# Kernel tuning notes

Measured on AMD Instinct MI355X. Metric: run time of the kernel, lower is better.

The kernel has to match this reference:

```python
import jax, jax.numpy as jnp
import numpy as np

B_BATCH, H_DIM, W_DIM, D_MODEL, N_STATE = 4, 64, 64, 512, 8


def setup_inputs() -> dict:
    key = jax.random.key(0)
    ks = jax.random.split(key, 7)
    x = jax.random.normal(ks[0], (B_BATCH, H_DIM * W_DIM, D_MODEL), jnp.float32)
    # stable diagonal recurrence: 0 < A < 1
    A = jax.random.uniform(ks[1], (D_MODEL, N_STATE), jnp.float32, 0.5, 0.99)
    Bm = jax.random.normal(ks[2], (D_MODEL, N_STATE), jnp.float32) * 0.1
    Cm = jax.random.normal(ks[3], (D_MODEL, N_STATE), jnp.float32) * 0.1
    D_skip = jax.random.normal(ks[4], (D_MODEL,), jnp.float32)
    Wp = jax.random.normal(ks[5], (D_MODEL, D_MODEL), jnp.float32) / np.sqrt(D_MODEL)
    b_proj = jnp.zeros((D_MODEL,), jnp.float32)
    return {"x": x, "h": H_DIM, "w": W_DIM, "A": A, "Bm": Bm, "Cm": Cm,
            "D_skip": D_skip, "Wp": Wp, "b_proj": b_proj}


def _ssm(xs, A, Bm, Cm, D_skip):
    # xs: (batch', L, d). Diagonal SSM: s_t = A*s_{t-1} + B*x_t; y_t = C.s_t + D*x_t
    bt, L, d = xs.shape
    n = A.shape[1]

    def step(s, x_t):  # s: (bt, d, n), x_t: (bt, d)
        s = A * s + Bm * x_t[:, :, None]
        y = jnp.einsum('bdn,dn->bd', s, Cm) + D_skip * x_t
        return s, y

    s0 = jnp.zeros((bt, d, n), xs.dtype)
    _, ys = jax.lax.scan(step, s0, jnp.swapaxes(xs, 0, 1))  # ys: (L, bt, d)
    return jnp.swapaxes(ys, 0, 1)


def reference(x, h, w, A, Bm, Cm, D_skip, Wp, b_proj):
    b, l, d = x.shape
    xg = x.reshape(b, h, w, d)
    # horizontal direction: 'b (h w) d -> (b w) h d' -> scan over h
    x_h = jnp.transpose(xg, (0, 2, 1, 3)).reshape(b * w, h, d)
    y_h = _ssm(x_h, A, Bm, Cm, D_skip).reshape(b, w, h, d)
    y_h = jnp.transpose(y_h, (0, 2, 1, 3)).reshape(b, l, d)
    # vertical direction: 'b (h w) d -> (b h) w d' -> scan over w
    x_v = xg.reshape(b * h, w, d)
    y_v = _ssm(x_v, A, Bm, Cm, D_skip).reshape(b, l, d)
    # fused add + output projection (Linear: x @ W.T + b)
    return (y_h + y_v) @ Wp.T + b_proj
```

## Files before the change

### kernel.cpp

```cpp
#include <hip/hip_runtime.h>

#define BB 4
#define HH 64
#define WW 64
#define DD 512
#define NS 8
#define MROWS (BB * HH * WW)

typedef __attribute__((ext_vector_type(8))) __bf16 bf16x8;
typedef __attribute__((ext_vector_type(4))) float f32x4;

__device__ inline short f2bf(float f) {
  unsigned u = __float_as_uint(f);
  return (short)((u + 0x7fff + ((u >> 16) & 1)) >> 16);
}
__device__ inline float bf2f(short s) {
  return __uint_as_float(((unsigned)(unsigned short)s) << 16);
}

__device__ inline float ssm_step(float xv, float* s, const float* a,
                                 const float* bm, const float* cm, float dk) {
#pragma unroll
  for (int n = 0; n < NS; ++n) s[n] = fmaf(a[n], s[n], bm[n] * xv);
  float p0 = s[0] * cm[0], p1 = s[1] * cm[1], p2 = s[2] * cm[2],
        p3 = s[3] * cm[3], p4 = s[4] * cm[4], p5 = s[5] * cm[5],
        p6 = s[6] * cm[6], p7 = s[7] * cm[7];
  float q0 = p0 + p1, q1 = p2 + p3, q2 = p4 + p5, q3 = p6 + p7;
  return fmaf(dk, xv, (q0 + q1) + (q2 + q3));
}

__global__ __launch_bounds__(256) void scan_h_kernel(
    const float* __restrict__ x, const float* __restrict__ A,
    const float* __restrict__ Bm, const float* __restrict__ Cm,
    const float* __restrict__ Dsk, short* __restrict__ y,
    const float* __restrict__ Wp, short* __restrict__ wb) {
  if (blockIdx.x >= 256) {
    const int cid = (blockIdx.x - 256) * 2 + blockIdx.y;
    const int i = (cid * 256 + (int)threadIdx.x) * 8;
    const float4 v0 = *(const float4*)&Wp[i];
    const float4 v1 = *(const float4*)&Wp[i + 4];
    short r[8];
    r[0] = f2bf(v0.x); r[1] = f2bf(v0.y); r[2] = f2bf(v0.z); r[3] = f2bf(v0.w);
    r[4] = f2bf(v1.x); r[5] = f2bf(v1.y); r[6] = f2bf(v1.z); r[7] = f2bf(v1.w);
    *(short4*)&wb[i] = *(short4*)&r[0];
    *(short4*)&wb[i + 4] = *(short4*)&r[4];
    return;
  }

  const int seq = blockIdx.x;
  const int d = blockIdx.y * 256 + threadIdx.x;
  const int b = seq >> 6;
  const int r = seq & 63;

  size_t base = ((size_t)b * HH * WW + r) * DD + d;
  const size_t step = (size_t)WW * DD;

  float a[NS], bm[NS], cm[NS], s[NS];
#pragma unroll
  for (int i = 0; i < NS; i += 4) {
    float4 t;
    t = *(const float4*)&A[(size_t)d * NS + i];
    a[i] = t.x; a[i + 1] = t.y; a[i + 2] = t.z; a[i + 3] = t.w;
    t = *(const float4*)&Bm[(size_t)d * NS + i];
    bm[i] = t.x; bm[i + 1] = t.y; bm[i + 2] = t.z; bm[i + 3] = t.w;
    t = *(const float4*)&Cm[(size_t)d * NS + i];
    cm[i] = t.x; cm[i + 1] = t.y; cm[i + 2] = t.z; cm[i + 3] = t.w;
  }
  const float dk = Dsk[d];
#pragma unroll
  for (int i = 0; i < NS; ++i) s[i] = 0.f;

  float xs[4][8];
#pragma unroll
  for (int i = 0; i < 8; ++i) xs[0][i] = x[base + (size_t)i * step];
#pragma unroll
  for (int i = 0; i < 8; ++i) xs[1][i] = x[base + (size_t)(8 + i) * step];

#pragma unroll 4
  for (int c = 0; c < 8; ++c) {
    const int cur = c & 3;
    if (c < 6) {
      const size_t pbase = base + 16 * step;
#pragma unroll
      for (int i = 0; i < 8; ++i)
        xs[(c + 2) & 3][i] = x[pbase + (size_t)i * step];
    }
#pragma unroll
    for (int i = 0; i < 8; ++i)
      y[base + (size_t)i * step] = f2bf(ssm_step(xs[cur][i], s, a, bm, cm, dk));
    base += 8 * step;
  }
}

__global__ __launch_bounds__(512) void scanv_gemm_kernel(
    const float* __restrict__ x, const float* __restrict__ A,
    const float* __restrict__ Bm, const float* __restrict__ Cm,
    const float* __restrict__ Dsk, const short* __restrict__ yh,
    const short* __restrict__ Wb, const float* __restrict__ bias,
    float* __restrict__ out) {
  __shared__ __align__(16) char LDSBUF[131072];
  short* Ys = (short*)LDSBUF;
  short* Bs0 = (short*)(LDSBUF + 65536);
  short* Bs1 = (short*)(LDSBUF + 98304);

  const int tid = (int)threadIdx.x;
  const int lane = tid & 63;
  const int wid = tid >> 6;
  const int m0 = blockIdx.x * 64;
  const int d = tid;

  auto stageB = [&](int ks, short* bsb) {
    const int k0 = ks * 32;
#pragma unroll
    for (int c = 0; c < 4; ++c) {
      const int chunk = wid * 4 + c;
      const int n = chunk * 16 + (lane >> 2);
      const int kslot = ((lane & 3) ^ (n & 3)) << 3;
      const short* g = &Wb[(size_t)n * DD + k0 + kslot];
      __builtin_amdgcn_global_load_lds(
          (const __attribute__((address_space(1))) unsigned int*)g,
          (__attribute__((address_space(3))) unsigned int*)((char*)bsb +
                                                            chunk * 1024),
          16, 0, 0);
    }
  };

  float a[NS], bm[NS], cm[NS], s[NS];
#pragma unroll
  for (int i = 0; i < NS; i += 4) {
    float4 t;
    t = *(const float4*)&A[(size_t)d * NS + i];
    a[i] = t.x; a[i + 1] = t.y; a[i + 2] = t.z; a[i + 3] = t.w;
    t = *(const float4*)&Bm[(size_t)d * NS + i];
    bm[i] = t.x; bm[i + 1] = t.y; bm[i + 2] = t.z; bm[i + 3] = t.w;
    t = *(const float4*)&Cm[(size_t)d * NS + i];
    cm[i] = t.x; cm[i + 1] = t.y; cm[i + 2] = t.z; cm[i + 3] = t.w;
  }
  const float dk = Dsk[d];
#pragma unroll
  for (int i = 0; i < NS; ++i) s[i] = 0.f;

  size_t base = (size_t)m0 * DD + d;
  stageB(0, Bs0);

  float xs[4][8], yp[4][8];
#pragma unroll
  for (int i = 0; i < 8; ++i) xs[0][i] = x[base + (size_t)i * DD];
#pragma unroll
  for (int i = 0; i < 8; ++i) yp[0][i] = bf2f(yh[base + (size_t)i * DD]);
#pragma unroll
  for (int i = 0; i < 8; ++i) xs[1][i] = x[base + (size_t)(8 + i) * DD];
#pragma unroll
  for (int i = 0; i < 8; ++i) yp[1][i] = bf2f(yh[base + (size_t)(8 + i) * DD]);

#pragma unroll 4
  for (int c = 0; c < 8; ++c) {
    const int cur = c & 3;
    if (c < 6) {
      const size_t pbase = base + 16 * DD;
#pragma unroll
      for (int i = 0; i < 8; ++i)
        xs[(c + 2) & 3][i] = x[pbase + (size_t)i * DD];
#pragma unroll
      for (int i = 0; i < 8; ++i)
        yp[(c + 2) & 3][i] = bf2f(yh[pbase + (size_t)i * DD]);
    }
#pragma unroll
    for (int i = 0; i < 8; ++i) {
      const int w = c * 8 + i;
      const float acc = ssm_step(xs[cur][i], s, a, bm, cm, dk) + yp[cur][i];
      Ys[w * DD + (d ^ ((w & 7) << 3))] = f2bf(acc);
    }
    base += 8 * DD;
  }

  __syncthreads();

  f32x4 acc4[4][4];
#pragma unroll
  for (int m = 0; m < 4; ++m)
#pragma unroll
    for (int n = 0; n < 4; ++n) acc4[m][n] = (f32x4){0.f, 0.f, 0.f, 0.f};

  const int fr = lane & 15;
  const int kfr = (lane >> 4) * 8;

  int cur = 0;
  for (int ks = 0; ks < 16; ++ks) {
    if (ks < 15) {
      stageB(ks + 1, (cur ^ 1) ? Bs1 : Bs0);
      asm volatile("s_waitcnt vmcnt(4)" ::: "memory");
    } else {
      asm volatile("s_waitcnt vmcnt(0)" ::: "memory");
    }
    __builtin_amdgcn_sched_barrier(0);

    const short* bsr = cur ? Bs1 : Bs0;
    bf16x8 af[4], bfv[4];
    const int kg = ks * 32 + kfr;
#pragma unroll
    for (int m = 0; m < 4; ++m) {
      const int r = m * 16 + fr;
      af[m] = *(const bf16x8*)(const void*)&Ys[r * DD + (kg ^ ((r & 7) << 3))];
    }
#pragma unroll
    for (int n = 0; n < 4; ++n) {
      const int nn = wid * 64 + n * 16 + fr;
      bfv[n] = *(const bf16x8*)(const void*)&bsr[nn * 32 +
                                                 (kfr ^ ((nn & 3) << 3))];
    }
    __builtin_amdgcn_s_setprio(1);
#pragma unroll
    for (int m = 0; m < 4; ++m)
#pragma unroll
      for (int n = 0; n < 4; ++n)
        acc4[m][n] = __builtin_amdgcn_mfma_f32_16x16x32_bf16(
            af[m], bfv[n], acc4[m][n], 0, 0, 0);
    __builtin_amdgcn_s_setprio(0);
    __builtin_amdgcn_sched_barrier(0);
    cur ^= 1;
  }

  __syncthreads();
  float* Wt = (float*)(LDSBUF + (size_t)wid * 16384);

  const int c16 = lane & 15;
  float bv[4];
#pragma unroll
  for (int n = 0; n < 4; ++n) bv[n] = bias[wid * 64 + n * 16 + c16];

#pragma unroll
  for (int m = 0; m < 4; ++m)
#pragma unroll
    for (int n = 0; n < 4; ++n)
#pragma unroll
      for (int j = 0; j < 4; ++j) {
        const int row = m * 16 + (lane >> 4) * 4 + j;
        const int col = n * 16 + c16;
        Wt[row * 64 + col] = acc4[m][n][j] + bv[n];
      }
#pragma unroll
  for (int rr = 0; rr < 16; ++rr) {
    const int row = rr * 4 + (lane >> 4);
    const int col4 = c16 * 4;
    const float4 v = *(const float4*)&Wt[row * 64 + col4];
    *(float4*)&out[(size_t)(m0 + row) * DD + wid * 64 + col4] = v;
  }
}

extern "C" void kernel_launch(void* const* d_in, const int* in_sizes, int n_in,
                              void* d_out, int out_size, void* d_ws,
                              size_t ws_size, hipStream_t stream) {
  const float* x = (const float*)d_in[0];
  const float* A = (const float*)d_in[3];
  const float* Bm = (const float*)d_in[4];
  const float* Cm = (const float*)d_in[5];
  const float* Dsk = (const float*)d_in[6];
  const float* Wp = (const float*)d_in[7];
  const float* bpj = (const float*)d_in[8];
  float* out = (float*)d_out;

  short* yh = (short*)d_ws;
  short* wb = (short*)((char*)d_ws + (size_t)MROWS * DD * 2);

  const dim3 grid_h(256 + 64, DD / 256);
  scan_h_kernel<<<grid_h, 256, 0, stream>>>(x, A, Bm, Cm, Dsk, yh, Wp, wb);

  scanv_gemm_kernel<<<BB * HH, 512, 0, stream>>>(x, A, Bm, Cm, Dsk, yh, wb,
                                                 bpj, out);
}
```

Baseline: 42.33 us.

## Split vertical scan into two halves with carry correction, double block threads

The fused vertical-scan+GEMM kernel now runs 1024 threads per block. Two thread groups each scan half of the 64-step row from a zero state. The second half is then corrected by adding C·(A^k·s_carry) from the first group's final state, passed through LDS. This halves the serial scan latency per block. The GEMM is re-tiled so each of 16 waves computes 64x32 outputs, and results are stored directly to global without the LDS transpose. The costs are an extra correction pass, a second bf16 rounding of the affected Ys entries, and uncoalesced scalar output stores. The priority hints are also removed.

```diff
diff --git a/kernel.cpp b/kernel.cpp
--- a/kernel.cpp
+++ b/kernel.cpp
@@ -92,7 +92,7 @@
   }
 }
 
-__global__ __launch_bounds__(512) void scanv_gemm_kernel(
+__global__ __launch_bounds__(1024) void scanv_gemm_kernel(
     const float* __restrict__ x, const float* __restrict__ A,
     const float* __restrict__ Bm, const float* __restrict__ Cm,
     const float* __restrict__ Dsk, const short* __restrict__ yh,
@@ -102,18 +102,20 @@
   short* Ys = (short*)LDSBUF;
   short* Bs0 = (short*)(LDSBUF + 65536);
   short* Bs1 = (short*)(LDSBUF + 98304);
+  float* sA = (float*)(LDSBUF + 98304);
 
   const int tid = (int)threadIdx.x;
   const int lane = tid & 63;
   const int wid = tid >> 6;
+  const int grp = tid >> 9;
+  const int d = tid & 511;
   const int m0 = blockIdx.x * 64;
-  const int d = tid;
 
   auto stageB = [&](int ks, short* bsb) {
     const int k0 = ks * 32;
 #pragma unroll
-    for (int c = 0; c < 4; ++c) {
-      const int chunk = wid * 4 + c;
+    for (int c = 0; c < 2; ++c) {
+      const int chunk = wid * 2 + c;
       const int n = chunk * 16 + (lane >> 2);
       const int kslot = ((lane & 3) ^ (n & 3)) << 3;
       const short* g = &Wb[(size_t)n * DD + k0 + kslot];
@@ -140,63 +142,84 @@
 #pragma unroll
   for (int i = 0; i < NS; ++i) s[i] = 0.f;
 
-  size_t base = (size_t)m0 * DD + d;
   stageB(0, Bs0);
 
-  float xs[4][8], yp[4][8];
+  size_t base = (size_t)m0 * DD + (size_t)(grp * 32) * DD + d;
+  float xs[2][8], yp[2][8];
 #pragma unroll
   for (int i = 0; i < 8; ++i) xs[0][i] = x[base + (size_t)i * DD];
 #pragma unroll
   for (int i = 0; i < 8; ++i) yp[0][i] = bf2f(yh[base + (size_t)i * DD]);
-#pragma unroll
-  for (int i = 0; i < 8; ++i) xs[1][i] = x[base + (size_t)(8 + i) * DD];
-#pragma unroll
-  for (int i = 0; i < 8; ++i) yp[1][i] = bf2f(yh[base + (size_t)(8 + i) * DD]);
-
-#pragma unroll 4
-  for (int c = 0; c < 8; ++c) {
-    const int cur = c & 3;
-    if (c < 6) {
-      const size_t pbase = base + 16 * DD;
-#pragma unroll
-      for (int i = 0; i < 8; ++i)
-        xs[(c + 2) & 3][i] = x[pbase + (size_t)i * DD];
-#pragma unroll
-      for (int i = 0; i < 8; ++i)
-        yp[(c + 2) & 3][i] = bf2f(yh[pbase + (size_t)i * DD]);
+
+#pragma unroll 2
+  for (int c = 0; c < 4; ++c) {
+    const int cur = c & 1, nxt = cur ^ 1;
+    const size_t nbase = base + 8 * DD;
+    if (c < 3) {
+#pragma unroll
+      for (int i = 0; i < 8; ++i) xs[nxt][i] = x[nbase + (size_t)i * DD];
+#pragma unroll
+      for (int i = 0; i < 8; ++i) yp[nxt][i] = bf2f(yh[nbase + (size_t)i * DD]);
     }
 #pragma unroll
     for (int i = 0; i < 8; ++i) {
-      const int w = c * 8 + i;
+      const int w = grp * 32 + c * 8 + i;
       const float acc = ssm_step(xs[cur][i], s, a, bm, cm, dk) + yp[cur][i];
       Ys[w * DD + (d ^ ((w & 7) << 3))] = f2bf(acc);
     }
-    base += 8 * DD;
-  }
-
+    base = nbase;
+  }
+
+  if (grp == 0) {
+#pragma unroll
+    for (int n = 0; n < NS; ++n) sA[n * 512 + d] = s[n];
+  }
   __syncthreads();
 
-  f32x4 acc4[4][4];
+  if (grp == 1) {
+    float ap[NS], sv[NS];
+#pragma unroll
+    for (int n = 0; n < NS; ++n) {
+      sv[n] = sA[n * 512 + d];
+      ap[n] = a[n];
+    }
+#pragma unroll 4
+    for (int w = 32; w < 64; ++w) {
+      float p0 = (cm[0] * ap[0]) * sv[0], p1 = (cm[1] * ap[1]) * sv[1],
+            p2 = (cm[2] * ap[2]) * sv[2], p3 = (cm[3] * ap[3]) * sv[3],
+            p4 = (cm[4] * ap[4]) * sv[4], p5 = (cm[5] * ap[5]) * sv[5],
+            p6 = (cm[6] * ap[6]) * sv[6], p7 = (cm[7] * ap[7]) * sv[7];
+      const float corr = ((p0 + p1) + (p2 + p3)) + ((p4 + p5) + (p6 + p7));
+      const int idx = w * DD + (d ^ ((w & 7) << 3));
+      Ys[idx] = f2bf(bf2f(Ys[idx]) + corr);
+#pragma unroll
+      for (int n = 0; n < NS; ++n) ap[n] *= a[n];
+    }
+  }
+  __syncthreads();
+
+  f32x4 acc4[4][2];
 #pragma unroll
   for (int m = 0; m < 4; ++m)
 #pragma unroll
-    for (int n = 0; n < 4; ++n) acc4[m][n] = (f32x4){0.f, 0.f, 0.f, 0.f};
+    for (int n = 0; n < 2; ++n) acc4[m][n] = (f32x4){0.f, 0.f, 0.f, 0.f};
 
   const int fr = lane & 15;
   const int kfr = (lane >> 4) * 8;
+  const int nc0 = wid * 32;
 
   int cur = 0;
   for (int ks = 0; ks < 16; ++ks) {
     if (ks < 15) {
       stageB(ks + 1, (cur ^ 1) ? Bs1 : Bs0);
-      asm volatile("s_waitcnt vmcnt(4)" ::: "memory");
+      asm volatile("s_waitcnt vmcnt(2)" ::: "memory");
     } else {
       asm volatile("s_waitcnt vmcnt(0)" ::: "memory");
     }
     __builtin_amdgcn_sched_barrier(0);
 
     const short* bsr = cur ? Bs1 : Bs0;
-    bf16x8 af[4], bfv[4];
+    bf16x8 af[4], bfv[2];
     const int kg = ks * 32 + kfr;
 #pragma unroll
     for (int m = 0; m < 4; ++m) {
@@ -204,47 +227,36 @@
       af[m] = *(const bf16x8*)(const void*)&Ys[r * DD + (kg ^ ((r & 7) << 3))];
     }
 #pragma unroll
-    for (int n = 0; n < 4; ++n) {
-      const int nn = wid * 64 + n * 16 + fr;
+    for (int n = 0; n < 2; ++n) {
+      const int nn = nc0 + n * 16 + fr;
       bfv[n] = *(const bf16x8*)(const void*)&bsr[nn * 32 +
                                                  (kfr ^ ((nn & 3) << 3))];
     }
-    __builtin_amdgcn_s_setprio(1);
 #pragma unroll
     for (int m = 0; m < 4; ++m)
 #pragma unroll
-      for (int n = 0; n < 4; ++n)
+      for (int n = 0; n < 2; ++n)
         acc4[m][n] = __builtin_amdgcn_mfma_f32_16x16x32_bf16(
             af[m], bfv[n], acc4[m][n], 0, 0, 0);
-    __builtin_amdgcn_s_setprio(0);
     __builtin_amdgcn_sched_barrier(0);
     cur ^= 1;
   }
 
-  __syncthreads();
-  float* Wt = (float*)(LDSBUF + (size_t)wid * 16384);
-
   const int c16 = lane & 15;
-  float bv[4];
-#pragma unroll
-  for (int n = 0; n < 4; ++n) bv[n] = bias[wid * 64 + n * 16 + c16];
-
-#pragma unroll
-  for (int m = 0; m < 4; ++m)
-#pragma unroll
-    for (int n = 0; n < 4; ++n)
-#pragma unroll
-      for (int j = 0; j < 4; ++j) {
-        const int row = m * 16 + (lane >> 4) * 4 + j;
-        const int col = n * 16 + c16;
-        Wt[row * 64 + col] = acc4[m][n][j] + bv[n];
-      }
-#pragma unroll
-  for (int rr = 0; rr < 16; ++rr) {
-    const int row = rr * 4 + (lane >> 4);
-    const int col4 = c16 * 4;
-    const float4 v = *(const float4*)&Wt[row * 64 + col4];
-    *(float4*)&out[(size_t)(m0 + row) * DD + wid * 64 + col4] = v;
+  const int r4 = (lane >> 4) * 4;
+  float bv[2];
+#pragma unroll
+  for (int n = 0; n < 2; ++n) bv[n] = bias[nc0 + n * 16 + c16];
+#pragma unroll
+  for (int m = 0; m < 4; ++m) {
+    const int rowb = m0 + m * 16 + r4;
+#pragma unroll
+    for (int n = 0; n < 2; ++n) {
+      const int col = nc0 + n * 16 + c16;
+#pragma unroll
+      for (int j = 0; j < 4; ++j)
+        out[(size_t)(rowb + j) * DD + col] = acc4[m][n][j] + bv[n];
+    }
   }
 }
 
@@ -266,6 +278,6 @@
   const dim3 grid_h(256 + 64, DD / 256);
   scan_h_kernel<<<grid_h, 256, 0, stream>>>(x, A, Bm, Cm, Dsk, yh, Wp, wb);
 
-  scanv_gemm_kernel<<<BB * HH, 512, 0, stream>>>(x, A, Bm, Cm, Dsk, yh, wb,
-                                                 bpj, out);
-}
+  scanv_gemm_kernel<<<BB * HH, 1024, 0, stream>>>(x, A, Bm, Cm, Dsk, yh, wb,
+                                                  bpj, out);
+}
```

Result: slower. 44.10 us (+4.2%).
